# Kernel optimization log

Hardware: AMD Instinct MI355X
Metric: run time of the kernel (lower is better)

Reference implementation:

```python
import jax, jax.numpy as jnp
import numpy as np

SCALES = (2, 4, 8)  # primitive_scales, one per branch


def setup_inputs() -> dict:
    key = jax.random.key(0)
    k0, k1, k2, k3, k4 = jax.random.split(key, 5)
    B, C, H, W = 16, 256, 128, 128
    s = 1.0 / np.sqrt(C).astype(np.float32)
    return {
        "x": jax.random.normal(k0, (B, C, H, W), jnp.float32),
        "W_proto": jax.random.normal(k1, (3, C, C), jnp.float32) * s,
        "W_frame": jax.random.normal(k2, (3, C, C), jnp.float32) * s,
        "W_out": jax.random.normal(k3, (3, C, C), jnp.float32) * s,
        "W_fuse": jax.random.normal(k4, (C, 3 * C), jnp.float32) * (1.0 / np.sqrt(3 * C).astype(np.float32)),
    }


def _branch(x, Wp, Wf, Wo, P):
    # x: [B,C,H,W]; adaptive_avg_pool2d(x, (H, P)) with W % P == 0 == mean over equal bins along W
    B, C, H, W = x.shape
    proto = x.reshape(B, C, H, P, W // P).mean(axis=-1)        # [B,C,H,P]
    proto = jnp.einsum('oc,bchp->bohp', Wp, proto)             # proto_proj (1x1 conv)
    q = jnp.einsum('oc,bchw->bhwo', Wf, x)                     # frame_proj + permute -> [B,H,W,C]
    # att = q @ k, k = proto.permute(0,2,1,3) -> [B,H,C,P]
    att = jnp.einsum('bhwc,bchp->bhwp', q, proto) * (1.0 / jnp.sqrt(jnp.float32(C)))
    att = jax.nn.softmax(att, axis=-1)                         # [B,H,W,P]
    # v = proto.permute(0,2,3,1) -> [B,H,P,C]; msg = att @ v -> [B,H,W,C]
    msg = jnp.einsum('bhwp,bchp->bhwc', att, proto)
    return jnp.einsum('oc,bhwc->bohw', Wo, msg)                # out_proj -> [B,C,H,W]


def reference(x, W_proto, W_frame, W_out, W_fuse):
    outs = [_branch(x, W_proto[i], W_frame[i], W_out[i], SCALES[i]) for i in range(len(SCALES))]
    cat = jnp.concatenate(outs, axis=1)                        # [B, 3C, H, W]
    return jnp.einsum('oc,bchw->bohw', W_fuse, cat) + x
```

## Files before the change

### kernel.cpp

```cpp
#include <hip/hip_runtime.h>
#include <hip/hip_bf16.h>
#include <math.h>

#define CC   256
#define HW   (128*128)
#define MAT  (CC*CC)
#define NBH  2048
#define N0   4096
#define N1   8192
#define N2   16384

typedef __attribute__((ext_vector_type(8))) short bf16x8;
typedef __attribute__((ext_vector_type(4))) float f32x4;

__global__ __launch_bounds__(256) void k_mats1(
    const float* __restrict__ Wp, const float* __restrict__ Wf,
    const float* __restrict__ Wo, const float* __restrict__ Wfu,
    __hip_bfloat16* __restrict__ A, float* __restrict__ E)
{
    int idx = blockIdx.x;
    int t = threadIdx.x;
    if (idx < 3*CC) {
        int i = idx >> 8, c = idx & 255;
        const float* wf = Wf + (size_t)i*MAT;
        const float* wp = Wp + (size_t)i*MAT;
        float acc = 0.f;
        for (int o = 0; o < CC; ++o)
            acc += wf[o*CC + c] * wp[o*CC + t];
        A[(size_t)i*512*CC + (size_t)c*CC + t] = __float2bfloat16(acc);
    } else {
        idx -= 3*CC;
        int i = idx >> 8, o = idx & 255;
        const float* wo = Wo + (size_t)i*MAT;
        const float* wfu = Wfu + (size_t)o*(3*CC) + i*CC;
        float acc = 0.f;
        for (int c3 = 0; c3 < CC; ++c3)
            acc += wfu[c3] * wo[c3*CC + t];
        E[(size_t)i*MAT + (size_t)o*CC + t] = acc;
    }
}

__global__ __launch_bounds__(256) void k_mats2(
    const float* __restrict__ Wp, const float* __restrict__ E,
    __hip_bfloat16* __restrict__ A)
{
    int idx = blockIdx.x;
    int i = idx >> 8, o = idx & 255;
    int t = threadIdx.x;
    const float* e = E + (size_t)i*MAT + (size_t)o*CC;
    const float* wp = Wp + (size_t)i*MAT;
    float acc = 0.f;
    for (int c = 0; c < CC; ++c)
        acc += e[c] * wp[c*CC + t];
    A[(size_t)i*512*CC + (size_t)(256+o)*CC + t] = __float2bfloat16(acc);
}

__global__ __launch_bounds__(256) void k_poolA(
    const float* __restrict__ x, float* __restrict__ binsG)
{
    int bc = blockIdx.x;
    int t = threadIdx.x;
    const float4* xp = (const float4*)(x + (size_t)bc*HW);
    __shared__ float bins[128][9];
    int hb = t >> 5;
    int bin = (t & 31) >> 2;
    #pragma unroll 4
    for (int i = 0; i < 16; ++i) {
        float4 v = xp[i*256 + t];
        float s = v.x + v.y + v.z + v.w;
        s += __shfl_xor(s, 1);
        s += __shfl_xor(s, 2);
        if ((t & 3) == 0) bins[i*8 + hb][bin] = s;
    }
    __syncthreads();
    int h = t >> 1, b0 = (t & 1) * 4;
    float4 o;
    o.x = bins[h][b0+0]; o.y = bins[h][b0+1];
    o.z = bins[h][b0+2]; o.w = bins[h][b0+3];
    ((float4*)binsG)[(size_t)bc*256 + t] = o;
}

__global__ __launch_bounds__(256) void k_poolB(
    const float* __restrict__ binsG, __hip_bfloat16* __restrict__ Bt)
{
    int bh = blockIdx.x;
    int b = bh >> 7, h = bh & 127;
    int c = threadIdx.x;
    const float* g = binsG + (((size_t)b*256 + c)*128 + h)*8;
    float4 lo = *(const float4*)(g);
    float4 hi = *(const float4*)(g + 4);
    float b8[8] = {lo.x, lo.y, lo.z, lo.w, hi.x, hi.y, hi.z, hi.w};

    __hip_bfloat16* B0 = Bt;
    __hip_bfloat16* B1 = Bt + (size_t)N0*CC;
    __hip_bfloat16* B2 = Bt + (size_t)(N0+N1)*CC;
    B0[((size_t)bh*2 + 0)*CC + c] = __float2bfloat16((b8[0]+b8[1]+b8[2]+b8[3]) * (1.f/64.f));
    B0[((size_t)bh*2 + 1)*CC + c] = __float2bfloat16((b8[4]+b8[5]+b8[6]+b8[7]) * (1.f/64.f));
    #pragma unroll
    for (int j = 0; j < 4; ++j)
        B1[((size_t)bh*4 + j)*CC + c] = __float2bfloat16((b8[2*j]+b8[2*j+1]) * (1.f/32.f));
    #pragma unroll
    for (int j = 0; j < 8; ++j)
        B2[((size_t)bh*8 + j)*CC + c] = __float2bfloat16(b8[j] * (1.f/16.f));
}

__global__ __launch_bounds__(128) void k_gemm(
    const __hip_bfloat16* __restrict__ A,
    const __hip_bfloat16* __restrict__ Bt,
    float* __restrict__ Cc)
{
    int blk = blockIdx.x;
    int br, lb, LP, poff;
    if (blk < 256)      { br = 0; lb = blk;       LP = 1; poff = 0; }
    else if (blk < 768) { br = 1; lb = blk - 256; LP = 2; poff = 2; }
    else                { br = 2; lb = blk - 768; LP = 3; poff = 6; }
    size_t aoff  = (size_t)br*512*CC;
    size_t btoff = (br == 0) ? 0 : (br == 1 ? (size_t)N0*CC : (size_t)(N0+N1)*CC);
    const __hip_bfloat16* Ab = A  + aoff;
    const __hip_bfloat16* Bb = Bt + btoff;

    int rb = lb & 3, cb = lb >> 2;
    int wv = threadIdx.x >> 6, lane = threadIdx.x & 63;
    int row0 = rb*128 + wv*64;
    int col0 = cb*64;
    int lr = lane & 15, lk = (lane >> 4) * 8;

    f32x4 acc[4][4] = {};
    for (int kk = 0; kk < CC; kk += 32) {
        bf16x8 af[4], bfr[4];
        #pragma unroll
        for (int m = 0; m < 4; ++m)
            af[m] = *reinterpret_cast<const bf16x8*>(Ab + (size_t)(row0 + m*16 + lr)*CC + kk + lk);
        #pragma unroll
        for (int n = 0; n < 4; ++n)
            bfr[n] = *reinterpret_cast<const bf16x8*>(Bb + (size_t)(col0 + n*16 + lr)*CC + kk + lk);
        #pragma unroll
        for (int m = 0; m < 4; ++m)
            #pragma unroll
            for (int n = 0; n < 4; ++n)
                acc[m][n] = __builtin_amdgcn_mfma_f32_16x16x32_bf16(af[m], bfr[n], acc[m][n], 0, 0, 0);
    }

    int cr = (lane >> 4) * 4, ccol = lane & 15;
    int pm = (1 << LP) - 1;
    #pragma unroll
    for (int m = 0; m < 4; ++m) {
        #pragma unroll
        for (int n = 0; n < 4; ++n) {
            int colg = col0 + n*16 + ccol;
            int bh = colg >> LP, p = colg & pm;
            float* dst = Cc + (size_t)bh*8192 + poff + p;
            #pragma unroll
            for (int j = 0; j < 4; ++j) {
                int r = row0 + m*16 + cr + j;
                dst[r*16] = acc[m][n][j];
            }
        }
    }
}

template<int L>
__device__ __forceinline__ void softmax2(float2* a) {
    float mx = a[0].x, my = a[0].y;
    #pragma unroll
    for (int j = 1; j < L; ++j) { mx = fmaxf(mx, a[j].x); my = fmaxf(my, a[j].y); }
    float sx = 0.f, sy = 0.f;
    #pragma unroll
    for (int j = 0; j < L; ++j) {
        a[j].x = __expf(a[j].x - mx); sx += a[j].x;
        a[j].y = __expf(a[j].y - my); sy += a[j].y;
    }
    float rx = 1.f / sx, ry = 1.f / sy;
    #pragma unroll
    for (int j = 0; j < L; ++j) { a[j].x *= rx; a[j].y *= ry; }
}

__global__ __launch_bounds__(256) void k_main(
    const float* __restrict__ x, const float* __restrict__ Cc,
    float* __restrict__ out)
{
    int bh = blockIdx.x;
    int b = bh >> 7, h = bh & 127;
    int t = threadIdx.x;
    int lane = t & 63;
    int wv = __builtin_amdgcn_readfirstlane(t >> 6);
    const float* Cb = Cc + (size_t)bh * 8192;
    size_t base2 = (((size_t)b*CC)*HW + (size_t)h*128) >> 1;
    const float2* x2 = (const float2*)x;
    float2* out2 = (float2*)out;
    __shared__ float2 att_s[4][64][14];

    float2 att[14];
    #pragma unroll
    for (int p = 0; p < 14; ++p) att[p] = make_float2(0.f, 0.f);

    #pragma unroll 8
    for (int cc = 0; cc < 64; ++cc) {
        int c = cc*4 + wv;
        float2 xv = x2[base2 + (size_t)c*(HW/2) + lane];
        const float* mp = Cb + c*16;
        #pragma unroll
        for (int p = 0; p < 14; ++p) {
            att[p].x += xv.x * mp[p];
            att[p].y += xv.y * mp[p];
        }
    }

    #pragma unroll
    for (int p = 0; p < 14; ++p) att_s[wv][lane][p] = att[p];
    __syncthreads();
    if (wv == 0) {
        #pragma unroll
        for (int p = 0; p < 14; ++p) {
            float2 a1 = att_s[1][lane][p], a2 = att_s[2][lane][p], a3 = att_s[3][lane][p];
            att[p].x = (att[p].x + a1.x + a2.x + a3.x) * 0.0625f;
            att[p].y = (att[p].y + a1.y + a2.y + a3.y) * 0.0625f;
        }
        softmax2<2>(att + 0);
        softmax2<4>(att + 2);
        softmax2<8>(att + 6);
        #pragma unroll
        for (int p = 0; p < 14; ++p) att_s[0][lane][p] = att[p];
    }
    __syncthreads();
    #pragma unroll
    for (int p = 0; p < 14; ++p) att[p] = att_s[0][lane][p];

    #pragma unroll 8
    for (int oo = 0; oo < 64; ++oo) {
        int o = oo*4 + wv;
        float2 xv = x2[base2 + (size_t)o*(HW/2) + lane];
        const float* vp = Cb + (256 + o)*16;
        float2 acc = xv;
        #pragma unroll
        for (int p = 0; p < 14; ++p) {
            acc.x += att[p].x * vp[p];
            acc.y += att[p].y * vp[p];
        }
        out2[base2 + (size_t)o*(HW/2) + lane] = acc;
    }
}

extern "C" void kernel_launch(void* const* d_in, const int* in_sizes, int n_in,
                              void* d_out, int out_size, void* d_ws, size_t ws_size,
                              hipStream_t stream)
{
    (void)in_sizes; (void)n_in; (void)out_size; (void)ws_size;
    const float* x   = (const float*)d_in[0];
    const float* Wp  = (const float*)d_in[1];
    const float* Wf  = (const float*)d_in[2];
    const float* Wo  = (const float*)d_in[3];
    const float* Wfu = (const float*)d_in[4];
    float* out = (float*)d_out;

    char* wsb = (char*)d_ws;
    float*          E     = (float*)wsb;
    __hip_bfloat16* A     = (__hip_bfloat16*)(wsb + 786432);
    __hip_bfloat16* Bt    = (__hip_bfloat16*)(wsb + 1572864);
    float*          Cc    = (float*)(wsb + 16252928);
    float*          binsG = Cc;

    k_mats1<<<dim3(6*CC),  dim3(256), 0, stream>>>(Wp, Wf, Wo, Wfu, A, E);
    k_mats2<<<dim3(3*CC),  dim3(256), 0, stream>>>(Wp, E, A);
    k_poolA<<<dim3(4096),  dim3(256), 0, stream>>>(x, binsG);
    k_poolB<<<dim3(NBH),   dim3(256), 0, stream>>>(binsG, Bt);
    k_gemm <<<dim3(1792),  dim3(128), 0, stream>>>(A, Bt, Cc);
    k_main <<<dim3(NBH),   dim3(256), 0, stream>>>(x, Cc, out);
}
```

Before: 342.3 us.

## Restructure k_main to one pixel per thread with two-way channel split

The main fused kernel now gives each thread a single W-pixel and splits the channel reduction across only two waves instead of four, where before each thread handled two pixels. This halves the per-thread attention registers, and the kernel adds a launch-bounds occupancy hint of 6. The cross-wave reduction shrinks from three partial sums to one, and the softmax is rewritten for scalars. In exchange, global loads become scalar 4-byte loads instead of float2, each thread makes more loop iterations, and the pooling kernel's unroll factor is raised.

```diff
diff --git a/kernel.cpp b/kernel.cpp
--- a/kernel.cpp
+++ b/kernel.cpp
@@ -64,7 +64,7 @@
     __shared__ float bins[128][9];
     int hb = t >> 5;
     int bin = (t & 31) >> 2;
-    #pragma unroll 4
+    #pragma unroll 8
     for (int i = 0; i < 16; ++i) {
         float4 v = xp[i*256 + t];
         float s = v.x + v.y + v.z + v.w;
@@ -160,22 +160,19 @@
 }
 
 template<int L>
-__device__ __forceinline__ void softmax2(float2* a) {
-    float mx = a[0].x, my = a[0].y;
-    #pragma unroll
-    for (int j = 1; j < L; ++j) { mx = fmaxf(mx, a[j].x); my = fmaxf(my, a[j].y); }
-    float sx = 0.f, sy = 0.f;
-    #pragma unroll
-    for (int j = 0; j < L; ++j) {
-        a[j].x = __expf(a[j].x - mx); sx += a[j].x;
-        a[j].y = __expf(a[j].y - my); sy += a[j].y;
-    }
-    float rx = 1.f / sx, ry = 1.f / sy;
-    #pragma unroll
-    for (int j = 0; j < L; ++j) { a[j].x *= rx; a[j].y *= ry; }
-}
-
-__global__ __launch_bounds__(256) void k_main(
+__device__ __forceinline__ void softmax_l(float* a) {
+    float m = a[0];
+    #pragma unroll
+    for (int j = 1; j < L; ++j) m = fmaxf(m, a[j]);
+    float s = 0.f;
+    #pragma unroll
+    for (int j = 0; j < L; ++j) { a[j] = __expf(a[j] - m); s += a[j]; }
+    float r = 1.f / s;
+    #pragma unroll
+    for (int j = 0; j < L; ++j) a[j] *= r;
+}
+
+__global__ __launch_bounds__(256, 6) void k_main(
     const float* __restrict__ x, const float* __restrict__ Cc,
     float* __restrict__ out)
 {
@@ -184,60 +181,52 @@
     int t = threadIdx.x;
     int lane = t & 63;
     int wv = __builtin_amdgcn_readfirstlane(t >> 6);
+    int ww = wv >> 1;
+    int wc = wv & 1;
+    int w = ww*64 + lane;
     const float* Cb = Cc + (size_t)bh * 8192;
-    size_t base2 = (((size_t)b*CC)*HW + (size_t)h*128) >> 1;
-    const float2* x2 = (const float2*)x;
-    float2* out2 = (float2*)out;
-    __shared__ float2 att_s[4][64][14];
-
-    float2 att[14];
-    #pragma unroll
-    for (int p = 0; p < 14; ++p) att[p] = make_float2(0.f, 0.f);
+    size_t base = ((size_t)b*CC)*HW + (size_t)h*128 + w;
+    __shared__ float att_s[128][15];
+
+    float att[14];
+    #pragma unroll
+    for (int p = 0; p < 14; ++p) att[p] = 0.f;
 
     #pragma unroll 8
-    for (int cc = 0; cc < 64; ++cc) {
-        int c = cc*4 + wv;
-        float2 xv = x2[base2 + (size_t)c*(HW/2) + lane];
+    for (int cc = 0; cc < 128; ++cc) {
+        int c = cc*2 + wc;
+        float xv = x[base + (size_t)c*HW];
         const float* mp = Cb + c*16;
         #pragma unroll
-        for (int p = 0; p < 14; ++p) {
-            att[p].x += xv.x * mp[p];
-            att[p].y += xv.y * mp[p];
-        }
-    }
-
-    #pragma unroll
-    for (int p = 0; p < 14; ++p) att_s[wv][lane][p] = att[p];
+        for (int p = 0; p < 14; ++p) att[p] += xv * mp[p];
+    }
+
+    if (wc == 1) {
+        #pragma unroll
+        for (int p = 0; p < 14; ++p) att_s[w][p] = att[p];
+    }
     __syncthreads();
-    if (wv == 0) {
-        #pragma unroll
-        for (int p = 0; p < 14; ++p) {
-            float2 a1 = att_s[1][lane][p], a2 = att_s[2][lane][p], a3 = att_s[3][lane][p];
-            att[p].x = (att[p].x + a1.x + a2.x + a3.x) * 0.0625f;
-            att[p].y = (att[p].y + a1.y + a2.y + a3.y) * 0.0625f;
-        }
-        softmax2<2>(att + 0);
-        softmax2<4>(att + 2);
-        softmax2<8>(att + 6);
-        #pragma unroll
-        for (int p = 0; p < 14; ++p) att_s[0][lane][p] = att[p];
+    if (wc == 0) {
+        #pragma unroll
+        for (int p = 0; p < 14; ++p) att[p] = (att[p] + att_s[w][p]) * 0.0625f;
+        softmax_l<2>(att + 0);
+        softmax_l<4>(att + 2);
+        softmax_l<8>(att + 6);
+        #pragma unroll
+        for (int p = 0; p < 14; ++p) att_s[w][p] = att[p];
     }
     __syncthreads();
     #pragma unroll
-    for (int p = 0; p < 14; ++p) att[p] = att_s[0][lane][p];
+    for (int p = 0; p < 14; ++p) att[p] = att_s[w][p];
 
     #pragma unroll 8
-    for (int oo = 0; oo < 64; ++oo) {
-        int o = oo*4 + wv;
-        float2 xv = x2[base2 + (size_t)o*(HW/2) + lane];
+    for (int oo = 0; oo < 128; ++oo) {
+        int o = oo*2 + wc;
+        float acc = x[base + (size_t)o*HW];
         const float* vp = Cb + (256 + o)*16;
-        float2 acc = xv;
-        #pragma unroll
-        for (int p = 0; p < 14; ++p) {
-            acc.x += att[p].x * vp[p];
-            acc.y += att[p].y * vp[p];
-        }
-        out2[base2 + (size_t)o*(HW/2) + lane] = acc;
+        #pragma unroll
+        for (int p = 0; p < 14; ++p) acc += att[p] * vp[p];
+        out[base + (size_t)o*HW] = acc;
     }
 }
 
```

Measured after the change: 367.4 us. 7.3% more time.

## Stage x tile in LDS once in k_main and store Cc in bf16

Applied to the files above, without the earlier changes.

k_main now uses 512 threads and loads each (b,h) row's 256x128 x tile into LDS with global_load_lds. The loads are pipelined with staged vmcnt waits, so x is read from global memory once instead of twice across the attention and output passes. The intermediate Cc coefficients are written as bf16 by k_gemm and unpacked with bit shifts, which halves that traffic at some cost in precision. k_poolA also issues all 16 loads up front for more memory-level parallelism. The roughly 158KB of LDS per block limits occupancy to one block per CU.

```diff
diff --git a/kernel.cpp b/kernel.cpp
--- a/kernel.cpp
+++ b/kernel.cpp
@@ -1,6 +1,7 @@
 #include <hip/hip_runtime.h>
 #include <hip/hip_bf16.h>
 #include <math.h>
+#include <stdint.h>
 
 #define CC   256
 #define HW   (128*128)
@@ -12,6 +13,8 @@
 
 typedef __attribute__((ext_vector_type(8))) short bf16x8;
 typedef __attribute__((ext_vector_type(4))) float f32x4;
+typedef __attribute__((address_space(3))) uint32_t lds_u32_t;
+typedef __attribute__((address_space(1))) const uint32_t glb_u32_t;
 
 __global__ __launch_bounds__(256) void k_mats1(
     const float* __restrict__ Wp, const float* __restrict__ Wf,
@@ -55,19 +58,20 @@
     A[(size_t)i*512*CC + (size_t)(256+o)*CC + t] = __float2bfloat16(acc);
 }
 
-__global__ __launch_bounds__(256) void k_poolA(
+__global__ __launch_bounds__(256, 4) void k_poolA(
     const float* __restrict__ x, float* __restrict__ binsG)
 {
     int bc = blockIdx.x;
     int t = threadIdx.x;
-    const float4* xp = (const float4*)(x + (size_t)bc*HW);
+    const float4* xp = (const float4*)(x + (size_t)bc*HW) + t;
     __shared__ float bins[128][9];
-    int hb = t >> 5;
-    int bin = (t & 31) >> 2;
-    #pragma unroll 4
+    float4 v[16];
+    #pragma unroll
+    for (int i = 0; i < 16; ++i) v[i] = xp[i*256];
+    int hb = t >> 5, bin = (t & 31) >> 2;
+    #pragma unroll
     for (int i = 0; i < 16; ++i) {
-        float4 v = xp[i*256 + t];
-        float s = v.x + v.y + v.z + v.w;
+        float s = v[i].x + v[i].y + v[i].z + v[i].w;
         s += __shfl_xor(s, 1);
         s += __shfl_xor(s, 2);
         if ((t & 3) == 0) bins[i*8 + hb][bin] = s;
@@ -107,7 +111,7 @@
 __global__ __launch_bounds__(128) void k_gemm(
     const __hip_bfloat16* __restrict__ A,
     const __hip_bfloat16* __restrict__ Bt,
-    float* __restrict__ Cc)
+    __hip_bfloat16* __restrict__ Cc)
 {
     int blk = blockIdx.x;
     int br, lb, LP, poff;
@@ -149,11 +153,11 @@
         for (int n = 0; n < 4; ++n) {
             int colg = col0 + n*16 + ccol;
             int bh = colg >> LP, p = colg & pm;
-            float* dst = Cc + (size_t)bh*8192 + poff + p;
+            __hip_bfloat16* dst = Cc + (size_t)bh*8192 + poff + p;
             #pragma unroll
             for (int j = 0; j < 4; ++j) {
                 int r = row0 + m*16 + cr + j;
-                dst[r*16] = acc[m][n][j];
+                dst[r*16] = __float2bfloat16(acc[m][n][j]);
             }
         }
     }
@@ -175,8 +179,8 @@
     for (int j = 0; j < L; ++j) { a[j].x *= rx; a[j].y *= ry; }
 }
 
-__global__ __launch_bounds__(256) void k_main(
-    const float* __restrict__ x, const float* __restrict__ Cc,
+__global__ __launch_bounds__(512, 1) void k_main(
+    const float* __restrict__ x, const __hip_bfloat16* __restrict__ Cc,
     float* __restrict__ out)
 {
     int bh = blockIdx.x;
@@ -184,60 +188,106 @@
     int t = threadIdx.x;
     int lane = t & 63;
     int wv = __builtin_amdgcn_readfirstlane(t >> 6);
-    const float* Cb = Cc + (size_t)bh * 8192;
-    size_t base2 = (((size_t)b*CC)*HW + (size_t)h*128) >> 1;
-    const float2* x2 = (const float2*)x;
-    float2* out2 = (float2*)out;
-    __shared__ float2 att_s[4][64][14];
+    const uint32_t* Cb = (const uint32_t*)(Cc + (size_t)bh*8192);
+    const float* xg = x + ((size_t)b*CC)*HW + h*128;
+    float2* o2 = (float2*)out + ((size_t)b*CC)*(HW/2) + h*64 + lane;
+
+    __shared__ float  xlds[256][128];
+    __shared__ float2 red[4][64][15];
 
     float2 att[14];
     #pragma unroll
     for (int p = 0; p < 14; ++p) att[p] = make_float2(0.f, 0.f);
 
-    #pragma unroll 8
-    for (int cc = 0; cc < 64; ++cc) {
-        int c = cc*4 + wv;
-        float2 xv = x2[base2 + (size_t)c*(HW/2) + lane];
-        const float* mp = Cb + c*16;
+    const float* gsrc = xg + (size_t)(lane >> 5)*HW + (lane & 31)*4;
+
+    #pragma unroll
+    for (int j = 0; j < 16; ++j) {
+        int c0 = wv*32 + 2*j;
+        __builtin_amdgcn_global_load_lds(
+            (glb_u32_t*)(gsrc + (size_t)c0*HW),
+            (lds_u32_t*)&xlds[c0][0], 16, 0, 0);
+    }
+    __builtin_amdgcn_sched_barrier(0);
+
+    #define CONSA(J, VM)                                                    \
+        asm volatile("s_waitcnt vmcnt(" #VM ")" ::: "memory");              \
+        __builtin_amdgcn_sched_barrier(0);                                  \
+        {                                                                   \
+            const int c0 = wv*32 + 2*(J);                                   \
+            const uint32_t* wr0 = Cb + (size_t)c0*8;                        \
+            float2 x0 = *(const float2*)&xlds[c0][lane*2];                  \
+            float2 x1 = *(const float2*)&xlds[c0+1][lane*2];                \
+            _Pragma("unroll")                                               \
+            for (int p = 0; p < 7; ++p) {                                   \
+                uint32_t u0 = wr0[p], u1 = wr0[8+p];                        \
+                float a0 = __uint_as_float(u0 << 16);                       \
+                float b0 = __uint_as_float(u0 & 0xFFFF0000u);               \
+                float a1 = __uint_as_float(u1 << 16);                       \
+                float b1 = __uint_as_float(u1 & 0xFFFF0000u);               \
+                att[2*p].x   += x0.x*a0 + x1.x*a1;                          \
+                att[2*p].y   += x0.y*a0 + x1.y*a1;                          \
+                att[2*p+1].x += x0.x*b0 + x1.x*b1;                          \
+                att[2*p+1].y += x0.y*b0 + x1.y*b1;                          \
+            }                                                               \
+        }
+
+    CONSA(0, 15); CONSA(1, 14); CONSA(2, 13); CONSA(3, 12);
+    CONSA(4, 11); CONSA(5, 10); CONSA(6,  9); CONSA(7,  8);
+    CONSA(8,  7); CONSA(9,  6); CONSA(10, 5); CONSA(11, 4);
+    CONSA(12, 3); CONSA(13, 2); CONSA(14, 1); CONSA(15, 0);
+    #undef CONSA
+
+    if (wv >= 4) {
+        #pragma unroll
+        for (int p = 0; p < 14; ++p) red[wv-4][lane][p] = att[p];
+    }
+    __syncthreads();
+    if (wv < 4) {
         #pragma unroll
         for (int p = 0; p < 14; ++p) {
-            att[p].x += xv.x * mp[p];
-            att[p].y += xv.y * mp[p];
-        }
-    }
-
-    #pragma unroll
-    for (int p = 0; p < 14; ++p) att_s[wv][lane][p] = att[p];
+            float2 r = red[wv][lane][p];
+            att[p].x += r.x; att[p].y += r.y;
+        }
+    }
+    __syncthreads();
+    if (wv >= 1 && wv < 4) {
+        #pragma unroll
+        for (int p = 0; p < 14; ++p) red[wv][lane][p] = att[p];
+    }
     __syncthreads();
     if (wv == 0) {
         #pragma unroll
         for (int p = 0; p < 14; ++p) {
-            float2 a1 = att_s[1][lane][p], a2 = att_s[2][lane][p], a3 = att_s[3][lane][p];
-            att[p].x = (att[p].x + a1.x + a2.x + a3.x) * 0.0625f;
-            att[p].y = (att[p].y + a1.y + a2.y + a3.y) * 0.0625f;
+            float2 r1 = red[1][lane][p], r2 = red[2][lane][p], r3 = red[3][lane][p];
+            att[p].x = (att[p].x + r1.x + r2.x + r3.x) * 0.0625f;
+            att[p].y = (att[p].y + r1.y + r2.y + r3.y) * 0.0625f;
         }
         softmax2<2>(att + 0);
         softmax2<4>(att + 2);
         softmax2<8>(att + 6);
         #pragma unroll
-        for (int p = 0; p < 14; ++p) att_s[0][lane][p] = att[p];
-    }
-    __syncthreads();
-    #pragma unroll
-    for (int p = 0; p < 14; ++p) att[p] = att_s[0][lane][p];
+        for (int p = 0; p < 14; ++p) red[0][lane][p] = att[p];
+    }
+    __syncthreads();
+    #pragma unroll
+    for (int p = 0; p < 14; ++p) att[p] = red[0][lane][p];
 
     #pragma unroll 8
-    for (int oo = 0; oo < 64; ++oo) {
-        int o = oo*4 + wv;
-        float2 xv = x2[base2 + (size_t)o*(HW/2) + lane];
-        const float* vp = Cb + (256 + o)*16;
+    for (int jj = 0; jj < 32; ++jj) {
+        int ch = wv*32 + jj;
+        const uint32_t* wr = Cb + (size_t)(256 + ch)*8;
+        float2 xv = *(const float2*)&xlds[ch][lane*2];
         float2 acc = xv;
         #pragma unroll
-        for (int p = 0; p < 14; ++p) {
-            acc.x += att[p].x * vp[p];
-            acc.y += att[p].y * vp[p];
-        }
-        out2[base2 + (size_t)o*(HW/2) + lane] = acc;
+        for (int p = 0; p < 7; ++p) {
+            uint32_t u = wr[p];
+            float vlo = __uint_as_float(u << 16);
+            float vhi = __uint_as_float(u & 0xFFFF0000u);
+            acc.x += att[2*p].x * vlo + att[2*p+1].x * vhi;
+            acc.y += att[2*p].y * vlo + att[2*p+1].y * vhi;
+        }
+        o2[(size_t)ch * (HW/2)] = acc;
     }
 }
 
@@ -257,13 +307,13 @@
     float*          E     = (float*)wsb;
     __hip_bfloat16* A     = (__hip_bfloat16*)(wsb + 786432);
     __hip_bfloat16* Bt    = (__hip_bfloat16*)(wsb + 1572864);
-    float*          Cc    = (float*)(wsb + 16252928);
-    float*          binsG = Cc;
+    __hip_bfloat16* Cc    = (__hip_bfloat16*)(wsb + 16252928);
+    float*          binsG = (float*)(wsb + 16252928);
 
     k_mats1<<<dim3(6*CC),  dim3(256), 0, stream>>>(Wp, Wf, Wo, Wfu, A, E);
     k_mats2<<<dim3(3*CC),  dim3(256), 0, stream>>>(Wp, E, A);
     k_poolA<<<dim3(4096),  dim3(256), 0, stream>>>(x, binsG);
     k_poolB<<<dim3(NBH),   dim3(256), 0, stream>>>(binsG, Bt);
     k_gemm <<<dim3(1792),  dim3(128), 0, stream>>>(A, Bt, Cc);
-    k_main <<<dim3(NBH),   dim3(256), 0, stream>>>(x, Cc, out);
-}
+    k_main <<<dim3(NBH),   dim3(512), 0, stream>>>(x, Cc, out);
+}
```

New measurement: 390.7 us. +14.2%, slower.
